# Kernel tuning notes

Hardware: AMD Instinct MI355X
Metric: run time of the kernel (lower is better)

The kernel has to match this reference:

```python
import jax, jax.numpy as jnp
import numpy as np
from itertools import product

# Static config
B, H, W, C = 16, 64, 64, 256
WIN = 8            # window size (square)
SHIFT = 4          # cyclic shift
NH = 8             # heads
HD = C // NH       # head dim
N = WIN * WIN      # tokens per window
HIDDEN = 1024


def _rel_pos_index():
    coords = np.stack(np.meshgrid(np.arange(WIN), np.arange(WIN), indexing='ij'))  # (2,w,w)
    flat = coords.reshape(2, -1)                                   # (2,N)
    rel = flat[:, :, None] - flat[:, None, :]                      # (2,N,N)
    rel = rel.transpose(1, 2, 0).astype(np.int64)
    rel[..., 0] += WIN - 1
    rel[..., 1] += WIN - 1
    rel[..., 0] *= 2 * WIN - 1
    return rel.sum(-1)                                             # (N,N)


def _shift_mask():
    # additive mask (nW, N, N) with -100 across shift boundaries (generate_mask)
    img = np.zeros((H, W), dtype=np.float32)
    slices = [(slice(0, -WIN), slice(-WIN, -SHIFT), slice(-SHIFT, None))] * 2
    cnt = 0
    for sx, sy in product(*slices):
        img[sx, sy] = cnt
        cnt += 1
    mw = img.reshape(H // WIN, WIN, W // WIN, WIN).transpose(0, 2, 1, 3).reshape(-1, N)  # (nW,N)
    diff = mw[:, None, :] - mw[:, :, None]
    return np.where(diff != 0, -100.0, 0.0).astype(np.float32)     # (nW,N,N)


REL_IDX = jnp.asarray(_rel_pos_index())
MASK = jnp.asarray(_shift_mask())


def _layernorm(x, scale, bias, eps=1e-5):
    mu = jnp.mean(x, axis=-1, keepdims=True)
    var = jnp.mean(jnp.square(x - mu), axis=-1, keepdims=True)
    return (x - mu) * jax.lax.rsqrt(var + eps) * scale + bias


def setup_inputs() -> dict:
    key = jax.random.key(0)
    ks = jax.random.split(key, 8)
    s = lambda fan_in: 1.0 / np.sqrt(fan_in)
    return {
        'x': jax.random.normal(ks[0], (B, H, W, C), jnp.float32),
        'ln1_scale': jnp.ones((C,), jnp.float32),
        'ln1_bias': jnp.zeros((C,), jnp.float32),
        'qkv_w': jax.random.normal(ks[1], (3 * C, C), jnp.float32) * s(C),
        'qkv_b': jnp.zeros((3 * C,), jnp.float32),
        'proj_w': jax.random.normal(ks[2], (C, C), jnp.float32) * s(C),
        'proj_b': jnp.zeros((C,), jnp.float32),
        'rel_bias': jax.random.normal(ks[3], ((2 * WIN - 1) ** 2, NH), jnp.float32) * 0.02,
        'ln2_scale': jnp.ones((C,), jnp.float32),
        'ln2_bias': jnp.zeros((C,), jnp.float32),
        'mlp_w1': jax.random.normal(ks[4], (HIDDEN, C), jnp.float32) * s(C),
        'mlp_b1': jnp.zeros((HIDDEN,), jnp.float32),
        'mlp_w2': jax.random.normal(ks[5], (C, HIDDEN), jnp.float32) * s(HIDDEN),
        'mlp_b2': jnp.zeros((C,), jnp.float32),
    }


def reference(x, ln1_scale, ln1_bias, qkv_w, qkv_b, proj_w, proj_b, rel_bias,
              ln2_scale, ln2_bias, mlp_w1, mlp_b1, mlp_w2, mlp_b2):
    nWh, nWw = H // WIN, W // WIN
    nW = nWh * nWw

    shortcut = x
    h = _layernorm(x, ln1_scale, ln1_bias)
    # cyclic shift
    h = jnp.roll(h, shift=(-SHIFT, -SHIFT), axis=(1, 2))
    # window partition -> (B*nW, N, C)
    h = h.reshape(B, nWh, WIN, nWw, WIN, C).transpose(0, 1, 3, 2, 4, 5).reshape(B * nW, N, C)

    # qkv
    qkv = h @ qkv_w.T + qkv_b                                # (B*nW, N, 3C)
    qkv = qkv.reshape(B * nW, N, 3, NH, HD)
    q, k, v = qkv[:, :, 0], qkv[:, :, 1], qkv[:, :, 2]       # (B*nW, N, NH, HD)

    scale = 1.0 / np.sqrt(HD)
    attn = jnp.einsum('bnhd,bmhd->bhnm', q * scale, k)       # (B*nW, NH, N, N)
    attn = attn + rel_bias[REL_IDX].transpose(2, 0, 1)[None]  # rel-pos bias (NH,N,N)
    attn = attn.reshape(B, nW, NH, N, N) + MASK[None, :, None]
    attn = jax.nn.softmax(attn.reshape(B * nW, NH, N, N), axis=-1)

    out = jnp.einsum('bhnm,bmhd->bnhd', attn, v).reshape(B * nW, N, C)
    out = out @ proj_w.T + proj_b

    # window reverse + reverse shift
    out = out.reshape(B, nWh, nWw, WIN, WIN, C).transpose(0, 1, 3, 2, 4, 5).reshape(B, H, W, C)
    out = jnp.roll(out, shift=(SHIFT, SHIFT), axis=(1, 2))

    x = shortcut + out
    # MLP
    h2 = _layernorm(x, ln2_scale, ln2_bias)
    h2 = jax.nn.gelu(h2 @ mlp_w1.T + mlp_b1, approximate=False) @ mlp_w2.T + mlp_b2
    return x + h2
```

## Files before the change

### kernel.cpp

```cpp
#include <hip/hip_runtime.h>
#include <hip/hip_bf16.h>
#include <math.h>

#define AS1 __attribute__((address_space(1)))
#define AS3 __attribute__((address_space(3)))

typedef __bf16  bf16x8 __attribute__((ext_vector_type(8)));
typedef float   f32x4  __attribute__((ext_vector_type(4)));
typedef __hip_bfloat16 bf16;

__device__ __forceinline__ void gload_lds16(const void* g, void* l) {
  __builtin_amdgcn_global_load_lds((const AS1 void*)g, (AS3 void*)l, 16, 0, 0);
}

__global__ __launch_bounds__(256) void k_conv_weights(
    const float* __restrict__ qkvw, const float* __restrict__ projw,
    const float* __restrict__ w1, const float* __restrict__ w2,
    bf16* __restrict__ dst)
{
  int i = blockIdx.x * 256 + threadIdx.x;
  float v;
  if (i < 196608)       v = qkvw[i];
  else if (i < 262144)  v = projw[i - 196608];
  else if (i < 524288)  v = w1[i - 262144];
  else                  v = w2[i - 524288];
  dst[i] = __float2bfloat16(v);
}

__global__ __launch_bounds__(256) void k_build_btab(
    const float* __restrict__ rel_bias, float* __restrict__ btab)
{
  int i = blockIdx.x * 256 + threadIdx.x;
  int h = i >> 12, r = i & 4095, n = r >> 6, m = r & 63;
  int idx = ((n >> 3) - (m >> 3) + 7) * 15 + ((n & 7) - (m & 7) + 7);
  btab[i] = rel_bias[idx * 8 + h];
}

__global__ __launch_bounds__(256) void k_ln1_window(
    const float* __restrict__ x, const float* __restrict__ sc,
    const float* __restrict__ bi, bf16* __restrict__ hout)
{
  int t = blockIdx.x * 4 + (threadIdx.x >> 6);
  int lane = threadIdx.x & 63;
  int win = t >> 6, nn = t & 63;
  int b = win >> 6, ww = win & 63;
  int ry = ((ww >> 3) << 3) + (nn >> 3);
  int rx = ((ww & 7) << 3) + (nn & 7);
  int sy = (ry + 4) & 63, sx = (rx + 4) & 63;
  const float* src = x + ((size_t)(((b << 6) + sy) << 6) + sx) * 256;
  f32x4 v = *(const f32x4*)(src + lane * 4);
  float s = v[0] + v[1] + v[2] + v[3];
  #pragma unroll
  for (int o = 1; o < 64; o <<= 1) s += __shfl_xor(s, o);
  float mu = s * (1.0f / 256.0f);
  float d0 = v[0]-mu, d1 = v[1]-mu, d2 = v[2]-mu, d3 = v[3]-mu;
  float q = d0*d0 + d1*d1 + d2*d2 + d3*d3;
  #pragma unroll
  for (int o = 1; o < 64; o <<= 1) q += __shfl_xor(q, o);
  float rstd = rsqrtf(q * (1.0f / 256.0f) + 1e-5f);
  int c = lane * 4;
  union { bf16 h[4]; uint2 u; } pk;
  pk.h[0] = __float2bfloat16(d0 * rstd * sc[c+0] + bi[c+0]);
  pk.h[1] = __float2bfloat16(d1 * rstd * sc[c+1] + bi[c+1]);
  pk.h[2] = __float2bfloat16(d2 * rstd * sc[c+2] + bi[c+2]);
  pk.h[3] = __float2bfloat16(d3 * rstd * sc[c+3] + bi[c+3]);
  *(uint2*)(hout + (size_t)t * 256 + c) = pk.u;
}

__global__ __launch_bounds__(256) void k_ln2(
    const float* __restrict__ x1, const float* __restrict__ sc,
    const float* __restrict__ bi, bf16* __restrict__ out)
{
  int t = blockIdx.x * 4 + (threadIdx.x >> 6);
  int lane = threadIdx.x & 63;
  const float* src = x1 + (size_t)t * 256;
  f32x4 v = *(const f32x4*)(src + lane * 4);
  float s = v[0] + v[1] + v[2] + v[3];
  #pragma unroll
  for (int o = 1; o < 64; o <<= 1) s += __shfl_xor(s, o);
  float mu = s * (1.0f / 256.0f);
  float d0 = v[0]-mu, d1 = v[1]-mu, d2 = v[2]-mu, d3 = v[3]-mu;
  float q = d0*d0 + d1*d1 + d2*d2 + d3*d3;
  #pragma unroll
  for (int o = 1; o < 64; o <<= 1) q += __shfl_xor(q, o);
  float rstd = rsqrtf(q * (1.0f / 256.0f) + 1e-5f);
  int c = lane * 4;
  union { bf16 h[4]; uint2 u; } pk;
  pk.h[0] = __float2bfloat16(d0 * rstd * sc[c+0] + bi[c+0]);
  pk.h[1] = __float2bfloat16(d1 * rstd * sc[c+1] + bi[c+1]);
  pk.h[2] = __float2bfloat16(d2 * rstd * sc[c+2] + bi[c+2]);
  pk.h[3] = __float2bfloat16(d3 * rstd * sc[c+3] + bi[c+3]);
  *(uint2*)(out + (size_t)t * 256 + c) = pk.u;
}

template<int EPI>
__global__ __launch_bounds__(256, 2) void k_pipe_ar(
    const bf16* __restrict__ A, const bf16* __restrict__ Bw,
    const float* __restrict__ bias,
    float* __restrict__ Cf, bf16* __restrict__ Cb,
    const float* __restrict__ resid, int N)
{
  __shared__ __align__(16) char lds[49152];

  const int tid = threadIdx.x;
  const int wid = tid >> 6;
  const int lane = tid & 63;
  const int l15 = lane & 15, lh = lane >> 4;
  const int rowBase = blockIdx.x * 128 + wid * 32;
  const int NC = N >> 5;

  auto stage = [&](int c) {
    char* dst = lds + (c % 3) * 16384;
    const char* srcB = (const char*)Bw + (size_t)c * 32 * 512;
    #pragma unroll
    for (int i = 0; i < 4; ++i) {
      int off = (i * 256 + tid) * 16;
      int r = off >> 9, cb = off & 511;
      int csw = cb ^ ((r & 7) << 4);
      gload_lds16(srcB + (size_t)r * 512 + csw, dst + off);
    }
  };

  bf16x8 af[2][8];
  {
    const bf16* a0 = A + (size_t)(rowBase + l15) * 256 + lh * 8;
    #pragma unroll
    for (int kk = 0; kk < 8; ++kk) {
      af[0][kk] = *(const bf16x8*)(a0 + kk * 32);
      af[1][kk] = *(const bf16x8*)(a0 + 4096 + kk * 32);
    }
  }

  size_t ra0, ra1;
  #pragma unroll
  for (int m = 0; m < 2; ++m) {
    int row = rowBase + m * 16 + l15;
    size_t ra;
    if (EPI == 2) {
      int win = row >> 6, nn = row & 63;
      int b = win >> 6, ww = win & 63;
      int ry = ((ww >> 3) << 3) + (nn >> 3);
      int rx = ((ww & 7) << 3) + (nn & 7);
      int fy = (ry + 4) & 63, fx = (rx + 4) & 63;
      ra = ((size_t)(((b << 6) + fy) << 6) + fx) * 256;
    } else {
      ra = (size_t)row * N;
    }
    if (m == 0) ra0 = ra; else ra1 = ra;
  }

  const int cl = lh * 4;
  f32x4 bc0 = *(const f32x4*)(bias + cl);
  f32x4 bc1 = *(const f32x4*)(bias + cl + 16);
  f32x4 rc00, rc10, rc01, rc11;
  if (EPI == 2) {
    rc00 = *(const f32x4*)(resid + ra0 + cl);
    rc10 = *(const f32x4*)(resid + ra1 + cl);
    rc01 = *(const f32x4*)(resid + ra0 + cl + 16);
    rc11 = *(const f32x4*)(resid + ra1 + cl + 16);
  }
  stage(0);
  stage(1);
  asm volatile("s_waitcnt vmcnt(4)" ::: "memory");
  __builtin_amdgcn_sched_barrier(0);

  for (int c = 0; c < NC; ++c) {
    __builtin_amdgcn_s_barrier();
    __builtin_amdgcn_sched_barrier(0);

    f32x4 bn0, bn1, rn00, rn10, rn01, rn11;
    if (c + 1 < NC) {
      const int ncl = (c + 1) * 32 + cl;
      bn0 = *(const f32x4*)(bias + ncl);
      bn1 = *(const f32x4*)(bias + ncl + 16);
      if (EPI == 2) {
        rn00 = *(const f32x4*)(resid + ra0 + ncl);
        rn10 = *(const f32x4*)(resid + ra1 + ncl);
        rn01 = *(const f32x4*)(resid + ra0 + ncl + 16);
        rn11 = *(const f32x4*)(resid + ra1 + ncl + 16);
      }
    }
    if (c + 2 < NC) stage(c + 2);

    const char* buf = lds + (c % 3) * 16384;
    const int xr = (l15 & 7) << 4;
    f32x4 a00 = (f32x4){0.f,0.f,0.f,0.f};
    f32x4 a10 = (f32x4){0.f,0.f,0.f,0.f};
    f32x4 a01 = (f32x4){0.f,0.f,0.f,0.f};
    f32x4 a11 = (f32x4){0.f,0.f,0.f,0.f};
    #pragma unroll
    for (int kk = 0; kk < 8; ++kk) {
      const int ko = (kk * 64 + lh * 16) ^ xr;
      bf16x8 b0 = *(const bf16x8*)(buf + (size_t)l15 * 512 + ko);
      bf16x8 b1 = *(const bf16x8*)(buf + (size_t)(16 + l15) * 512 + ko);
      a00 = __builtin_amdgcn_mfma_f32_16x16x32_bf16(b0, af[0][kk], a00, 0, 0, 0);
      a10 = __builtin_amdgcn_mfma_f32_16x16x32_bf16(b0, af[1][kk], a10, 0, 0, 0);
      a01 = __builtin_amdgcn_mfma_f32_16x16x32_bf16(b1, af[0][kk], a01, 0, 0, 0);
      a11 = __builtin_amdgcn_mfma_f32_16x16x32_bf16(b1, af[1][kk], a11, 0, 0, 0);
    }

    const int colb0 = c * 32 + cl;
    const int colb1 = colb0 + 16;
    if (EPI == 0) {
      union { bf16 h[4]; uint2 u; } p;
      #pragma unroll
      for (int j = 0; j < 4; ++j) p.h[j] = __float2bfloat16(a00[j] + bc0[j]);
      *(uint2*)(Cb + ra0 + colb0) = p.u;
      #pragma unroll
      for (int j = 0; j < 4; ++j) p.h[j] = __float2bfloat16(a10[j] + bc0[j]);
      *(uint2*)(Cb + ra1 + colb0) = p.u;
      #pragma unroll
      for (int j = 0; j < 4; ++j) p.h[j] = __float2bfloat16(a01[j] + bc1[j]);
      *(uint2*)(Cb + ra0 + colb1) = p.u;
      #pragma unroll
      for (int j = 0; j < 4; ++j) p.h[j] = __float2bfloat16(a11[j] + bc1[j]);
      *(uint2*)(Cb + ra1 + colb1) = p.u;
    } else if (EPI == 1) {
      auto gelu = [](float v) {
        float w = fmaf(v * v, 0.1029434f, 2.3022083f);
        float e = __builtin_amdgcn_exp2f(-v * w);
        return v * __builtin_amdgcn_rcpf(1.0f + e);
      };
      union { bf16 h[4]; uint2 u; } p;
      #pragma unroll
      for (int j = 0; j < 4; ++j) p.h[j] = __float2bfloat16(gelu(a00[j] + bc0[j]));
      *(uint2*)(Cb + ra0 + colb0) = p.u;
      #pragma unroll
      for (int j = 0; j < 4; ++j) p.h[j] = __float2bfloat16(gelu(a10[j] + bc0[j]));
      *(uint2*)(Cb + ra1 + colb0) = p.u;
      #pragma unroll
      for (int j = 0; j < 4; ++j) p.h[j] = __float2bfloat16(gelu(a01[j] + bc1[j]));
      *(uint2*)(Cb + ra0 + colb1) = p.u;
      #pragma unroll
      for (int j = 0; j < 4; ++j) p.h[j] = __float2bfloat16(gelu(a11[j] + bc1[j]));
      *(uint2*)(Cb + ra1 + colb1) = p.u;
    } else {
      f32x4 o;
      #pragma unroll
      for (int j = 0; j < 4; ++j) o[j] = a00[j] + bc0[j] + rc00[j];
      *(f32x4*)(Cf + ra0 + colb0) = o;
      #pragma unroll
      for (int j = 0; j < 4; ++j) o[j] = a10[j] + bc0[j] + rc10[j];
      *(f32x4*)(Cf + ra1 + colb0) = o;
      #pragma unroll
      for (int j = 0; j < 4; ++j) o[j] = a01[j] + bc1[j] + rc01[j];
      *(f32x4*)(Cf + ra0 + colb1) = o;
      #pragma unroll
      for (int j = 0; j < 4; ++j) o[j] = a11[j] + bc1[j] + rc11[j];
      *(f32x4*)(Cf + ra1 + colb1) = o;
    }

    if (c + 1 < NC) {
      bc0 = bn0; bc1 = bn1;
      if (EPI == 2) { rc00 = rn00; rc10 = rn10; rc01 = rn01; rc11 = rn11; }
    }

    if (c + 1 < NC) {
      if (EPI == 2) {
        if (c > 0 && c + 2 < NC) { asm volatile("s_waitcnt vmcnt(18)" ::: "memory"); }
        else                     { asm volatile("s_waitcnt vmcnt(10)" ::: "memory"); }
      } else {
        if (c > 0 && c + 2 < NC) { asm volatile("s_waitcnt vmcnt(14)" ::: "memory"); }
        else                     { asm volatile("s_waitcnt vmcnt(6)"  ::: "memory"); }
      }
      __builtin_amdgcn_sched_barrier(0);
    }
  }
}

__global__ __launch_bounds__(256, 2) void k_pipe_bt(
    const bf16* __restrict__ A, const bf16* __restrict__ Bw,
    const float* __restrict__ bias, float* __restrict__ Cf)
{
  __shared__ __align__(16) char lds[73728];

  const int tid = threadIdx.x;
  const int wid = tid >> 6;
  const int lane = tid & 63;
  const int l15 = lane & 15, lh = lane >> 4;
  const int wr = (wid >> 1) * 64;
  const int wc = (wid & 1) * 128;
  const int rowBase = blockIdx.x * 128;

  auto stage = [&](int t) {
    char* dA = lds + (t % 3) * 24576;
    char* dB = dA + 8192;
    #pragma unroll
    for (int i = 0; i < 2; ++i) {
      int off = (i * 256 + tid) * 16;
      int r = off >> 6, cb = off & 63;
      int csw = cb ^ ((r & 3) << 4);
      gload_lds16((const char*)(A + (size_t)(rowBase + r) * 1024 + t * 32) + csw, dA + off);
    }
    #pragma unroll
    for (int i = 0; i < 4; ++i) {
      int off = (i * 256 + tid) * 16;
      int r = off >> 6, cb = off & 63;
      int csw = cb ^ ((r & 3) << 4);
      gload_lds16((const char*)(Bw + (size_t)r * 1024 + t * 32) + csw, dB + off);
    }
  };

  f32x4 acc[4][8];
  #pragma unroll
  for (int m = 0; m < 4; ++m)
    #pragma unroll
    for (int n = 0; n < 8; ++n) acc[m][n] = (f32x4){0.f,0.f,0.f,0.f};

  stage(0);
  stage(1);
  asm volatile("s_waitcnt vmcnt(6)" ::: "memory");
  __builtin_amdgcn_sched_barrier(0);

  for (int t = 0; t < 32; ++t) {
    __builtin_amdgcn_s_barrier();
    __builtin_amdgcn_sched_barrier(0);

    if (t + 2 < 32) stage(t + 2);

    const char* bufA = lds + (t % 3) * 24576;
    const char* bufB = bufA + 8192;
    bf16x8 af[4], bfr[8];
    #pragma unroll
    for (int m = 0; m < 4; ++m) {
      int rA = wr + m * 16 + l15;
      af[m] = *(const bf16x8*)(bufA + rA * 64 + ((lh * 16) ^ ((rA & 3) << 4)));
    }
    #pragma unroll
    for (int n = 0; n < 8; ++n) {
      int rB = wc + n * 16 + l15;
      bfr[n] = *(const bf16x8*)(bufB + rB * 64 + ((lh * 16) ^ ((rB & 3) << 4)));
    }
    #pragma unroll
    for (int m = 0; m < 4; ++m)
      #pragma unroll
      for (int n = 0; n < 8; ++n)
        acc[m][n] = __builtin_amdgcn_mfma_f32_16x16x32_bf16(bfr[n], af[m], acc[m][n], 0, 0, 0);

    if (t + 2 < 32) { asm volatile("s_waitcnt vmcnt(6)" ::: "memory"); }
    else if (t < 31) { asm volatile("s_waitcnt vmcnt(0)" ::: "memory"); }
    __builtin_amdgcn_sched_barrier(0);
  }

  #pragma unroll
  for (int m = 0; m < 4; ++m) {
    size_t rowAddr = (size_t)(rowBase + wr + m * 16 + l15) * 256;
    #pragma unroll
    for (int n = 0; n < 8; ++n) {
      const int colb = wc + n * 16 + lh * 4;
      const f32x4 b4 = *(const f32x4*)(bias + colb);
      f32x4* p = (f32x4*)(Cf + rowAddr + colb);
      f32x4 cc = *p;
      #pragma unroll
      for (int j = 0; j < 4; ++j) cc[j] += acc[m][n][j] + b4[j];
      *p = cc;
    }
  }
}

__global__ __launch_bounds__(256) void k_attn(
    const bf16* __restrict__ qkv, const float* __restrict__ btab,
    bf16* __restrict__ outp)
{
  __shared__ __align__(16) char smem[71680];
  float* sb = (float*)smem;
  const int tid = threadIdx.x, wid = tid >> 6, lane = tid & 63;
  const int l15 = lane & 15, lh = lane >> 4;
  const int h = blockIdx.x >> 8;
  const int win = ((blockIdx.x & 255) << 2) + wid;
  const int tb = win << 6;
  char* plw = smem + 16384 + wid * 9216;
  char* vtw = smem + 16384 + 36864 + wid * 4608;

  for (int i = tid; i < 4096; i += 256) sb[i] = btab[(h << 12) + i];
  __syncthreads();

  bf16x8 qf[4], kf[4];
  #pragma unroll
  for (int m = 0; m < 4; ++m) {
    size_t base = (size_t)(tb + m * 16 + l15) * 768 + h * 32 + lh * 8;
    qf[m] = *(const bf16x8*)(qkv + base);
    kf[m] = *(const bf16x8*)(qkv + base + 256);
  }
  f32x4 s[4][4];
  #pragma unroll
  for (int i = 0; i < 4; ++i)
    #pragma unroll
    for (int j = 0; j < 4; ++j) {
      s[i][j] = (f32x4){0.f,0.f,0.f,0.f};
      s[i][j] = __builtin_amdgcn_mfma_f32_16x16x32_bf16(qf[i], kf[j], s[i][j], 0, 0, 0);
    }

  #pragma unroll
  for (int it = 0; it < 32; ++it) {
    int idx = it * 64 + lane;
    int m = idx >> 5, d = idx & 31;
    bf16 vv = qkv[(size_t)(tb + m) * 768 + 512 + h * 32 + d];
    *(bf16*)(vtw + d * 144 + m * 2) = vv;
  }

  int ww = win & 63, wi = ww >> 3, wj = ww & 7;
  int labm[4];
  #pragma unroll
  for (int jf = 0; jf < 4; ++jf) {
    int m = jf * 16 + l15;
    int yy = wi * 8 + (m >> 3), xx = wj * 8 + (m & 7);
    labm[jf] = (yy < 56 ? 0 : (yy < 60 ? 1 : 2)) * 3 + (xx < 56 ? 0 : (xx < 60 ? 1 : 2));
  }
  float rsum[4][4];
  const float scale = 0.17677669529663687f;
  #pragma unroll
  for (int i = 0; i < 4; ++i) {
    #pragma unroll
    for (int j = 0; j < 4; ++j) {
      int n = i * 16 + lh * 4 + j;
      int yy = wi * 8 + (n >> 3), xx = wj * 8 + (n & 7);
      int labn = (yy < 56 ? 0 : (yy < 60 ? 1 : 2)) * 3 + (xx < 56 ? 0 : (xx < 60 ? 1 : 2));
      float vals[4]; float mx = -1e30f;
      #pragma unroll
      for (int jf = 0; jf < 4; ++jf) {
        int m = jf * 16 + l15;
        float v = s[i][jf][j] * scale + sb[(n << 6) + m];
        if (labn != labm[jf]) v -= 100.0f;
        vals[jf] = v; mx = fmaxf(mx, v);
      }
      #pragma unroll
      for (int o = 1; o < 16; o <<= 1) mx = fmaxf(mx, __shfl_xor(mx, o));
      float sum = 0.0f;
      #pragma unroll
      for (int jf = 0; jf < 4; ++jf) {
        float e = __expf(vals[jf] - mx);
        sum += e;
        *(bf16*)(plw + n * 144 + (jf * 16 + l15) * 2) = __float2bfloat16(e);
      }
      #pragma unroll
      for (int o = 1; o < 16; o <<= 1) sum += __shfl_xor(sum, o);
      rsum[i][j] = sum;
    }
  }
  __syncthreads();

  f32x4 o[4][2];
  #pragma unroll
  for (int i = 0; i < 4; ++i) { o[i][0] = (f32x4){0.f,0.f,0.f,0.f}; o[i][1] = (f32x4){0.f,0.f,0.f,0.f}; }
  #pragma unroll
  for (int kk = 0; kk < 2; ++kk) {
    bf16x8 pf[4], vf[2];
    #pragma unroll
    for (int i = 0; i < 4; ++i)
      pf[i] = *(const bf16x8*)(plw + (i * 16 + l15) * 144 + kk * 64 + lh * 16);
    #pragma unroll
    for (int df = 0; df < 2; ++df)
      vf[df] = *(const bf16x8*)(vtw + (df * 16 + l15) * 144 + kk * 64 + lh * 16);
    #pragma unroll
    for (int i = 0; i < 4; ++i)
      #pragma unroll
      for (int df = 0; df < 2; ++df)
        o[i][df] = __builtin_amdgcn_mfma_f32_16x16x32_bf16(pf[i], vf[df], o[i][df], 0, 0, 0);
  }
  #pragma unroll
  for (int i = 0; i < 4; ++i)
    #pragma unroll
    for (int df = 0; df < 2; ++df)
      #pragma unroll
      for (int j = 0; j < 4; ++j) {
        int n = i * 16 + lh * 4 + j;
        int d = df * 16 + l15;
        float v = o[i][df][j] / rsum[i][j];
        outp[(size_t)(tb + n) * 256 + h * 32 + d] = __float2bfloat16(v);
      }
}

extern "C" void kernel_launch(void* const* d_in, const int* in_sizes, int n_in,
                              void* d_out, int out_size, void* d_ws, size_t ws_size,
                              hipStream_t stream) {
  (void)in_sizes; (void)n_in; (void)out_size; (void)ws_size;
  const float* x      = (const float*)d_in[0];
  const float* ln1_s  = (const float*)d_in[1];
  const float* ln1_b  = (const float*)d_in[2];
  const float* qkv_w  = (const float*)d_in[3];
  const float* qkv_b  = (const float*)d_in[4];
  const float* proj_w = (const float*)d_in[5];
  const float* proj_b = (const float*)d_in[6];
  const float* rel_b  = (const float*)d_in[7];
  const float* ln2_s  = (const float*)d_in[8];
  const float* ln2_b  = (const float*)d_in[9];
  const float* w1     = (const float*)d_in[10];
  const float* b1     = (const float*)d_in[11];
  const float* w2     = (const float*)d_in[12];
  const float* b2     = (const float*)d_in[13];

  char* ws = (char*)d_ws;
  bf16*  wqkv  = (bf16*)(ws + 0);
  bf16*  wproj = wqkv + 196608;
  bf16*  wm1   = wqkv + 262144;
  bf16*  wm2   = wqkv + 524288;
  float* btab  = (float*)(ws + 1572864);
  bf16*  hbuf  = (bf16*)(ws + 2097152);
  bf16*  qkvb  = (bf16*)(ws + 35651584);
  bf16*  attnb = (bf16*)(ws + 136314880);
  bf16*  ln2buf = hbuf;
  bf16*  actb  = qkvb;
  float* x1    = (float*)d_out;

  k_conv_weights<<<3072, 256, 0, stream>>>(qkv_w, proj_w, w1, w2, wqkv);
  k_build_btab<<<128, 256, 0, stream>>>(rel_b, btab);
  k_ln1_window<<<16384, 256, 0, stream>>>(x, ln1_s, ln1_b, hbuf);
  k_pipe_ar<0><<<512, 256, 0, stream>>>(hbuf, wqkv, qkv_b, nullptr, qkvb, nullptr, 768);
  k_attn<<<2048, 256, 0, stream>>>(qkvb, btab, attnb);
  k_pipe_ar<2><<<512, 256, 0, stream>>>(attnb, wproj, proj_b, x1, nullptr, x, 256);
  k_ln2<<<16384, 256, 0, stream>>>(x1, ln2_s, ln2_b, ln2buf);
  k_pipe_ar<1><<<512, 256, 0, stream>>>(ln2buf, wm1, b1, nullptr, actb, nullptr, 1024);
  k_pipe_bt<<<512, 256, 0, stream>>>(actb, wm2, b2, x1);
}
```

Measured before the change: 322.4 us.

## Fuse LayerNorm2 into proj GEMM epilogue, deepen B pipeline, coalesce bf16 stores

Removes the standalone LN2 kernel. The proj GEMM now accumulates per-row sum and sum-of-squares while it writes x1, then re-reads its own x1 rows to write the normalized bf16 output. The B-tile ring grows from three to four stages with adjusted vmcnt waits. Bf16 epilogues are staged through a per-wave LDS scratch so each lane writes 16-byte stores. The changes raise LDS use, which may cut occupancy, and the one-pass variance formula is less numerically robust.

```diff
diff --git a/kernel.cpp b/kernel.cpp
--- a/kernel.cpp
+++ b/kernel.cpp
@@ -67,40 +67,16 @@
   *(uint2*)(hout + (size_t)t * 256 + c) = pk.u;
 }
 
-__global__ __launch_bounds__(256) void k_ln2(
-    const float* __restrict__ x1, const float* __restrict__ sc,
-    const float* __restrict__ bi, bf16* __restrict__ out)
-{
-  int t = blockIdx.x * 4 + (threadIdx.x >> 6);
-  int lane = threadIdx.x & 63;
-  const float* src = x1 + (size_t)t * 256;
-  f32x4 v = *(const f32x4*)(src + lane * 4);
-  float s = v[0] + v[1] + v[2] + v[3];
-  #pragma unroll
-  for (int o = 1; o < 64; o <<= 1) s += __shfl_xor(s, o);
-  float mu = s * (1.0f / 256.0f);
-  float d0 = v[0]-mu, d1 = v[1]-mu, d2 = v[2]-mu, d3 = v[3]-mu;
-  float q = d0*d0 + d1*d1 + d2*d2 + d3*d3;
-  #pragma unroll
-  for (int o = 1; o < 64; o <<= 1) q += __shfl_xor(q, o);
-  float rstd = rsqrtf(q * (1.0f / 256.0f) + 1e-5f);
-  int c = lane * 4;
-  union { bf16 h[4]; uint2 u; } pk;
-  pk.h[0] = __float2bfloat16(d0 * rstd * sc[c+0] + bi[c+0]);
-  pk.h[1] = __float2bfloat16(d1 * rstd * sc[c+1] + bi[c+1]);
-  pk.h[2] = __float2bfloat16(d2 * rstd * sc[c+2] + bi[c+2]);
-  pk.h[3] = __float2bfloat16(d3 * rstd * sc[c+3] + bi[c+3]);
-  *(uint2*)(out + (size_t)t * 256 + c) = pk.u;
-}
-
 template<int EPI>
 __global__ __launch_bounds__(256, 2) void k_pipe_ar(
     const bf16* __restrict__ A, const bf16* __restrict__ Bw,
     const float* __restrict__ bias,
     float* __restrict__ Cf, bf16* __restrict__ Cb,
-    const float* __restrict__ resid, int N)
+    const float* __restrict__ resid,
+    const float* __restrict__ ln2s, const float* __restrict__ ln2b,
+    bf16* __restrict__ ln2out, int N)
 {
-  __shared__ __align__(16) char lds[49152];
+  __shared__ __align__(16) char lds[65536 + 10240];
 
   const int tid = threadIdx.x;
   const int wid = tid >> 6;
@@ -108,9 +84,10 @@
   const int l15 = lane & 15, lh = lane >> 4;
   const int rowBase = blockIdx.x * 128 + wid * 32;
   const int NC = N >> 5;
+  char* scr = lds + 65536 + wid * 2560;
 
   auto stage = [&](int c) {
-    char* dst = lds + (c % 3) * 16384;
+    char* dst = lds + (c & 3) * 16384;
     const char* srcB = (const char*)Bw + (size_t)c * 32 * 512;
     #pragma unroll
     for (int i = 0; i < 4; ++i) {
@@ -131,22 +108,24 @@
     }
   }
 
-  size_t ra0, ra1;
-  #pragma unroll
-  for (int m = 0; m < 2; ++m) {
-    int row = rowBase + m * 16 + l15;
-    size_t ra;
-    if (EPI == 2) {
-      int win = row >> 6, nn = row & 63;
-      int b = win >> 6, ww = win & 63;
-      int ry = ((ww >> 3) << 3) + (nn >> 3);
-      int rx = ((ww & 7) << 3) + (nn & 7);
-      int fy = (ry + 4) & 63, fx = (rx + 4) & 63;
-      ra = ((size_t)(((b << 6) + fy) << 6) + fx) * 256;
-    } else {
-      ra = (size_t)row * N;
-    }
-    if (m == 0) ra0 = ra; else ra1 = ra;
+  auto remap = [&](int row) -> size_t {
+    int win = row >> 6, nn = row & 63;
+    int b = win >> 6, ww = win & 63;
+    int ry = ((ww >> 3) << 3) + (nn >> 3);
+    int rx = ((ww & 7) << 3) + (nn & 7);
+    int fy = (ry + 4) & 63, fx = (rx + 4) & 63;
+    return ((size_t)(((b << 6) + fy) << 6) + fx) * 256;
+  };
+  size_t ra0 = 0, ra1 = 0;
+  size_t rbA, rbB;
+  if (EPI == 2) {
+    ra0 = remap(rowBase + l15);
+    ra1 = remap(rowBase + 16 + l15);
+    rbA = remap(rowBase + (lane >> 2));
+    rbB = remap(rowBase + 16 + (lane >> 2));
+  } else {
+    rbA = (size_t)(rowBase + (lane >> 2)) * N;
+    rbB = rbA + (size_t)16 * N;
   }
 
   const int cl = lh * 4;
@@ -159,10 +138,11 @@
     rc01 = *(const f32x4*)(resid + ra0 + cl + 16);
     rc11 = *(const f32x4*)(resid + ra1 + cl + 16);
   }
-  stage(0);
-  stage(1);
-  asm volatile("s_waitcnt vmcnt(4)" ::: "memory");
+  stage(0); stage(1); stage(2);
+  asm volatile("s_waitcnt vmcnt(8)" ::: "memory");
   __builtin_amdgcn_sched_barrier(0);
+
+  float s0 = 0.f, q0 = 0.f, s1 = 0.f, q1 = 0.f;
 
   for (int c = 0; c < NC; ++c) {
     __builtin_amdgcn_s_barrier();
@@ -180,10 +160,11 @@
         rn11 = *(const f32x4*)(resid + ra1 + ncl + 16);
       }
     }
-    if (c + 2 < NC) stage(c + 2);
-
-    const char* buf = lds + (c % 3) * 16384;
+    if (c + 3 < NC) stage(c + 3);
+
+    const char* buf = lds + (c & 3) * 16384;
     const int xr = (l15 & 7) << 4;
+    const int base0 = l15 * 512;
     f32x4 a00 = (f32x4){0.f,0.f,0.f,0.f};
     f32x4 a10 = (f32x4){0.f,0.f,0.f,0.f};
     f32x4 a01 = (f32x4){0.f,0.f,0.f,0.f};
@@ -191,63 +172,59 @@
     #pragma unroll
     for (int kk = 0; kk < 8; ++kk) {
       const int ko = (kk * 64 + lh * 16) ^ xr;
-      bf16x8 b0 = *(const bf16x8*)(buf + (size_t)l15 * 512 + ko);
-      bf16x8 b1 = *(const bf16x8*)(buf + (size_t)(16 + l15) * 512 + ko);
+      bf16x8 b0 = *(const bf16x8*)(buf + base0 + ko);
+      bf16x8 b1 = *(const bf16x8*)(buf + base0 + 8192 + ko);
       a00 = __builtin_amdgcn_mfma_f32_16x16x32_bf16(b0, af[0][kk], a00, 0, 0, 0);
       a10 = __builtin_amdgcn_mfma_f32_16x16x32_bf16(b0, af[1][kk], a10, 0, 0, 0);
       a01 = __builtin_amdgcn_mfma_f32_16x16x32_bf16(b1, af[0][kk], a01, 0, 0, 0);
       a11 = __builtin_amdgcn_mfma_f32_16x16x32_bf16(b1, af[1][kk], a11, 0, 0, 0);
     }
 
-    const int colb0 = c * 32 + cl;
-    const int colb1 = colb0 + 16;
-    if (EPI == 0) {
-      union { bf16 h[4]; uint2 u; } p;
-      #pragma unroll
-      for (int j = 0; j < 4; ++j) p.h[j] = __float2bfloat16(a00[j] + bc0[j]);
-      *(uint2*)(Cb + ra0 + colb0) = p.u;
-      #pragma unroll
-      for (int j = 0; j < 4; ++j) p.h[j] = __float2bfloat16(a10[j] + bc0[j]);
-      *(uint2*)(Cb + ra1 + colb0) = p.u;
-      #pragma unroll
-      for (int j = 0; j < 4; ++j) p.h[j] = __float2bfloat16(a01[j] + bc1[j]);
-      *(uint2*)(Cb + ra0 + colb1) = p.u;
-      #pragma unroll
-      for (int j = 0; j < 4; ++j) p.h[j] = __float2bfloat16(a11[j] + bc1[j]);
-      *(uint2*)(Cb + ra1 + colb1) = p.u;
-    } else if (EPI == 1) {
-      auto gelu = [](float v) {
-        float w = fmaf(v * v, 0.1029434f, 2.3022083f);
-        float e = __builtin_amdgcn_exp2f(-v * w);
-        return v * __builtin_amdgcn_rcpf(1.0f + e);
+    const int cbs = c * 32 + (lane & 3) * 8;
+    if (EPI == 0 || EPI == 1) {
+      auto cvt = [](float v) -> bf16 {
+        if (EPI == 1) {
+          float w = fmaf(v * v, 0.1029434f, 2.3022083f);
+          float e = __builtin_amdgcn_exp2f(-v * w);
+          v = v * __builtin_amdgcn_rcpf(1.0f + e);
+        }
+        return __float2bfloat16(v);
       };
-      union { bf16 h[4]; uint2 u; } p;
-      #pragma unroll
-      for (int j = 0; j < 4; ++j) p.h[j] = __float2bfloat16(gelu(a00[j] + bc0[j]));
-      *(uint2*)(Cb + ra0 + colb0) = p.u;
-      #pragma unroll
-      for (int j = 0; j < 4; ++j) p.h[j] = __float2bfloat16(gelu(a10[j] + bc0[j]));
-      *(uint2*)(Cb + ra1 + colb0) = p.u;
-      #pragma unroll
-      for (int j = 0; j < 4; ++j) p.h[j] = __float2bfloat16(gelu(a01[j] + bc1[j]));
-      *(uint2*)(Cb + ra0 + colb1) = p.u;
-      #pragma unroll
-      for (int j = 0; j < 4; ++j) p.h[j] = __float2bfloat16(gelu(a11[j] + bc1[j]));
-      *(uint2*)(Cb + ra1 + colb1) = p.u;
+      union { bf16 h[4]; uint2 u; } p00, p01, p10, p11;
+      #pragma unroll
+      for (int j = 0; j < 4; ++j) {
+        p00.h[j] = cvt(a00[j] + bc0[j]);
+        p01.h[j] = cvt(a01[j] + bc1[j]);
+        p10.h[j] = cvt(a10[j] + bc0[j]);
+        p11.h[j] = cvt(a11[j] + bc1[j]);
+      }
+      *(uint2*)(scr + l15 * 80 + lh * 8)            = p00.u;
+      *(uint2*)(scr + l15 * 80 + 32 + lh * 8)       = p01.u;
+      *(uint2*)(scr + (16 + l15) * 80 + lh * 8)     = p10.u;
+      *(uint2*)(scr + (16 + l15) * 80 + 32 + lh * 8)= p11.u;
+      uint4 r0 = *(const uint4*)(scr + (lane >> 2) * 80 + (lane & 3) * 16);
+      uint4 r1 = *(const uint4*)(scr + (16 + (lane >> 2)) * 80 + (lane & 3) * 16);
+      *(uint4*)(Cb + rbA + cbs) = r0;
+      *(uint4*)(Cb + rbB + cbs) = r1;
     } else {
-      f32x4 o;
-      #pragma unroll
-      for (int j = 0; j < 4; ++j) o[j] = a00[j] + bc0[j] + rc00[j];
-      *(f32x4*)(Cf + ra0 + colb0) = o;
-      #pragma unroll
-      for (int j = 0; j < 4; ++j) o[j] = a10[j] + bc0[j] + rc10[j];
-      *(f32x4*)(Cf + ra1 + colb0) = o;
-      #pragma unroll
-      for (int j = 0; j < 4; ++j) o[j] = a01[j] + bc1[j] + rc01[j];
-      *(f32x4*)(Cf + ra0 + colb1) = o;
-      #pragma unroll
-      for (int j = 0; j < 4; ++j) o[j] = a11[j] + bc1[j] + rc11[j];
-      *(f32x4*)(Cf + ra1 + colb1) = o;
+      const int colb0 = c * 32 + cl, colb1 = colb0 + 16;
+      f32x4 o00, o10, o01, o11;
+      #pragma unroll
+      for (int j = 0; j < 4; ++j) {
+        o00[j] = a00[j] + bc0[j] + rc00[j];
+        o10[j] = a10[j] + bc0[j] + rc10[j];
+        o01[j] = a01[j] + bc1[j] + rc01[j];
+        o11[j] = a11[j] + bc1[j] + rc11[j];
+      }
+      *(f32x4*)(Cf + ra0 + colb0) = o00;
+      *(f32x4*)(Cf + ra1 + colb0) = o10;
+      *(f32x4*)(Cf + ra0 + colb1) = o01;
+      *(f32x4*)(Cf + ra1 + colb1) = o11;
+      #pragma unroll
+      for (int j = 0; j < 4; ++j) {
+        s0 += o00[j] + o01[j];  q0 += o00[j]*o00[j] + o01[j]*o01[j];
+        s1 += o10[j] + o11[j];  q1 += o10[j]*o10[j] + o11[j]*o11[j];
+      }
     }
 
     if (c + 1 < NC) {
@@ -257,13 +234,54 @@
 
     if (c + 1 < NC) {
       if (EPI == 2) {
-        if (c > 0 && c + 2 < NC) { asm volatile("s_waitcnt vmcnt(18)" ::: "memory"); }
-        else                     { asm volatile("s_waitcnt vmcnt(10)" ::: "memory"); }
+        if (c == 0)            { asm volatile("s_waitcnt vmcnt(18)" ::: "memory"); }
+        else if (c + 3 < NC)   { asm volatile("s_waitcnt vmcnt(28)" ::: "memory"); }
+        else                   { asm volatile("s_waitcnt vmcnt(6)"  ::: "memory"); }
       } else {
-        if (c > 0 && c + 2 < NC) { asm volatile("s_waitcnt vmcnt(14)" ::: "memory"); }
-        else                     { asm volatile("s_waitcnt vmcnt(6)"  ::: "memory"); }
+        if (c == 0)            { asm volatile("s_waitcnt vmcnt(12)" ::: "memory"); }
+        else if (c + 3 < NC)   { asm volatile("s_waitcnt vmcnt(16)" ::: "memory"); }
+        else                   { asm volatile("s_waitcnt vmcnt(6)"  ::: "memory"); }
       }
       __builtin_amdgcn_sched_barrier(0);
+    }
+  }
+
+  if (EPI == 2) {
+    s0 += __shfl_xor(s0, 16); s0 += __shfl_xor(s0, 32);
+    q0 += __shfl_xor(q0, 16); q0 += __shfl_xor(q0, 32);
+    s1 += __shfl_xor(s1, 16); s1 += __shfl_xor(s1, 32);
+    q1 += __shfl_xor(q1, 16); q1 += __shfl_xor(q1, 32);
+    float mu0 = s0 * (1.0f / 256.0f);
+    float rs0 = rsqrtf(q0 * (1.0f / 256.0f) - mu0 * mu0 + 1e-5f);
+    float mu1 = s1 * (1.0f / 256.0f);
+    float rs1 = rsqrtf(q1 * (1.0f / 256.0f) - mu1 * mu1 + 1e-5f);
+    for (int c = 0; c < NC; ++c) {
+      const int cb0 = c * 32 + cl, cb1 = cb0 + 16;
+      f32x4 v00 = *(const f32x4*)(Cf + ra0 + cb0);
+      f32x4 v01 = *(const f32x4*)(Cf + ra0 + cb1);
+      f32x4 v10 = *(const f32x4*)(Cf + ra1 + cb0);
+      f32x4 v11 = *(const f32x4*)(Cf + ra1 + cb1);
+      f32x4 sa = *(const f32x4*)(ln2s + cb0);
+      f32x4 sb = *(const f32x4*)(ln2s + cb1);
+      f32x4 ba = *(const f32x4*)(ln2b + cb0);
+      f32x4 bb = *(const f32x4*)(ln2b + cb1);
+      union { bf16 h[4]; uint2 u; } p00, p01, p10, p11;
+      #pragma unroll
+      for (int j = 0; j < 4; ++j) {
+        p00.h[j] = __float2bfloat16((v00[j] - mu0) * rs0 * sa[j] + ba[j]);
+        p01.h[j] = __float2bfloat16((v01[j] - mu0) * rs0 * sb[j] + bb[j]);
+        p10.h[j] = __float2bfloat16((v10[j] - mu1) * rs1 * sa[j] + ba[j]);
+        p11.h[j] = __float2bfloat16((v11[j] - mu1) * rs1 * sb[j] + bb[j]);
+      }
+      *(uint2*)(scr + l15 * 80 + lh * 8)             = p00.u;
+      *(uint2*)(scr + l15 * 80 + 32 + lh * 8)        = p01.u;
+      *(uint2*)(scr + (16 + l15) * 80 + lh * 8)      = p10.u;
+      *(uint2*)(scr + (16 + l15) * 80 + 32 + lh * 8) = p11.u;
+      uint4 r0 = *(const uint4*)(scr + (lane >> 2) * 80 + (lane & 3) * 16);
+      uint4 r1 = *(const uint4*)(scr + (16 + (lane >> 2)) * 80 + (lane & 3) * 16);
+      const int cbs = c * 32 + (lane & 3) * 8;
+      *(uint4*)(ln2out + rbA + cbs) = r0;
+      *(uint4*)(ln2out + rbB + cbs) = r1;
     }
   }
 }
@@ -506,10 +524,12 @@
   k_conv_weights<<<3072, 256, 0, stream>>>(qkv_w, proj_w, w1, w2, wqkv);
   k_build_btab<<<128, 256, 0, stream>>>(rel_b, btab);
   k_ln1_window<<<16384, 256, 0, stream>>>(x, ln1_s, ln1_b, hbuf);
-  k_pipe_ar<0><<<512, 256, 0, stream>>>(hbuf, wqkv, qkv_b, nullptr, qkvb, nullptr, 768);
+  k_pipe_ar<0><<<512, 256, 0, stream>>>(hbuf, wqkv, qkv_b, nullptr, qkvb, nullptr,
+                                        nullptr, nullptr, nullptr, 768);
   k_attn<<<2048, 256, 0, stream>>>(qkvb, btab, attnb);
-  k_pipe_ar<2><<<512, 256, 0, stream>>>(attnb, wproj, proj_b, x1, nullptr, x, 256);
-  k_ln2<<<16384, 256, 0, stream>>>(x1, ln2_s, ln2_b, ln2buf);
-  k_pipe_ar<1><<<512, 256, 0, stream>>>(ln2buf, wm1, b1, nullptr, actb, nullptr, 1024);
+  k_pipe_ar<2><<<512, 256, 0, stream>>>(attnb, wproj, proj_b, x1, nullptr, x,
+                                        ln2_s, ln2_b, ln2buf, 256);
+  k_pipe_ar<1><<<512, 256, 0, stream>>>(ln2buf, wm1, b1, nullptr, actb, nullptr,
+                                        nullptr, nullptr, nullptr, 1024);
   k_pipe_bt<<<512, 256, 0, stream>>>(actb, wm2, b2, x1);
 }
```

New measurement: 309.4 us. 1.04x faster.
